# Kernel tuning notes

Measured on AMD Instinct MI355X. Metric: run time of the kernel, lower is better.

Reference implementation:

```python
import jax, jax.numpy as jnp
import numpy as np

B, L, D = 4, 256, 2048
LE, DE = 2048, 1024
H = 16
HD = D // H  # 128
ROPE_BASE = 10000.0


def apply_rope(q):
    # q: [B, H, L, HD]; rotate interleaved pairs along seq axis L (torchtune-style)
    half = HD // 2
    inv_freq = 1.0 / (ROPE_BASE ** (jnp.arange(0, HD, 2, dtype=jnp.float32) / HD))  # [half]
    pos = jnp.arange(L, dtype=jnp.float32)
    ang = pos[:, None] * inv_freq[None, :]           # [L, half]
    cos = jnp.cos(ang)[None, None, :, :]             # [1,1,L,half]
    sin = jnp.sin(ang)[None, None, :, :]
    qr = q.reshape(B, H, L, half, 2)
    q1, q2 = qr[..., 0], qr[..., 1]
    out = jnp.stack([q1 * cos - q2 * sin, q1 * sin + q2 * cos], axis=-1)
    return out.reshape(B, H, L, HD)


def setup_inputs() -> dict:
    key = jax.random.key(0)
    ks = jax.random.split(key, 7)
    s_d = 1.0 / np.sqrt(D)
    s_e = 1.0 / np.sqrt(DE)
    return {
        "x": jax.random.normal(ks[0], (B, L, D), jnp.float32),
        "encoder_inputs": jax.random.normal(ks[1], (B, LE, DE), jnp.float32),
        "Wq": jax.random.normal(ks[2], (D, D), jnp.float32) * s_d,
        "bq": jnp.zeros((D,), jnp.float32),
        "Wk": jax.random.normal(ks[3], (DE, D), jnp.float32) * s_e,
        "bk": jnp.zeros((D,), jnp.float32),
        "Wv": jax.random.normal(ks[4], (DE, D), jnp.float32) * s_e,
        "bv": jnp.zeros((D,), jnp.float32),
        "Wo": jax.random.normal(ks[5], (D, D), jnp.float32) * s_d,
        "bo": jnp.zeros((D,), jnp.float32),
    }


def reference(x, encoder_inputs, Wq, bq, Wk, bk, Wv, bv, Wo, bo):
    q = (x @ Wq + bq).reshape(B, L, H, HD).transpose(0, 2, 1, 3)              # [B,H,L,HD]
    k = (encoder_inputs @ Wk + bk).reshape(B, LE, H, HD).transpose(0, 2, 1, 3)  # [B,H,Le,HD]
    v = (encoder_inputs @ Wv + bv).reshape(B, LE, H, HD).transpose(0, 2, 1, 3)
    q = apply_rope(q)
    scale = 1.0 / jnp.sqrt(jnp.float32(HD))
    scores = jnp.einsum("bhld,bhmd->bhlm", q, k) * scale                      # [B,H,L,Le]
    attn = jax.nn.softmax(scores, axis=-1)
    ctx = jnp.einsum("bhlm,bhmd->bhld", attn, v)                              # [B,H,L,HD]
    ctx = ctx.transpose(0, 2, 1, 3).reshape(B, L, D)
    return ctx @ Wo + bo
```

## Files before the change

### kernel.cpp

```cpp
#include <hip/hip_runtime.h>


#define B_ 4
#define L_ 256
#define D_ 2048
#define LE_ 2048
#define DE_ 1024
#define H_ 16
#define HD_ 128

using f32x4  = __attribute__((ext_vector_type(4))) float;
using bf16x8 = __attribute__((ext_vector_type(8))) short;

__device__ __forceinline__ unsigned short f2bf(float f) {
    union { float f; unsigned int u; } v; v.f = f;
    unsigned int r = v.u + 0x7fffu + ((v.u >> 16) & 1u);
    return (unsigned short)(r >> 16);
}
__device__ __forceinline__ float b2f(unsigned short h) {
    union { unsigned int u; float f; } v; v.u = ((unsigned int)h) << 16;
    return v.f;
}

__device__ __forceinline__ void load_lds16(const void* g, void* l) {
    __builtin_amdgcn_global_load_lds((const __attribute__((address_space(1))) void*)g,
                                     (__attribute__((address_space(3))) void*)l, 16, 0, 0);
}

__global__ void cast_f32_bf16(const float* __restrict__ in, unsigned short* __restrict__ out, int n) {
    int i = (blockIdx.x * 256 + threadIdx.x) * 4;
    if (i < n) {
        float4 v = *(const float4*)(in + i);
        ushort4 o;
        o.x = f2bf(v.x); o.y = f2bf(v.y); o.z = f2bf(v.z); o.w = f2bf(v.w);
        *(ushort4*)(out + i) = o;
    }
}

__global__ void transpose_f32_bf16(const float* __restrict__ in, unsigned short* __restrict__ out,
                                   int R, int C) {
    __shared__ float t[32][33];
    int r0 = blockIdx.y * 32, c0 = blockIdx.x * 32;
    int tx = threadIdx.x, ty = threadIdx.y;
    #pragma unroll
    for (int i = 0; i < 32; i += 8) t[ty + i][tx] = in[(long)(r0 + ty + i) * C + c0 + tx];
    __syncthreads();
    #pragma unroll
    for (int i = 0; i < 32; i += 8) out[(long)(c0 + ty + i) * R + r0 + tx] = f2bf(t[tx][ty + i]);
}

__global__ void transpose_bf16_batched(const unsigned short* __restrict__ in,
                                       unsigned short* __restrict__ out, int R, int C) {
    __shared__ unsigned short t[32][33];
    long zo = (long)blockIdx.z * R * C;
    int r0 = blockIdx.y * 32, c0 = blockIdx.x * 32;
    int tx = threadIdx.x, ty = threadIdx.y;
    #pragma unroll
    for (int i = 0; i < 32; i += 8) t[ty + i][tx] = in[zo + (long)(r0 + ty + i) * C + c0 + tx];
    __syncthreads();
    #pragma unroll
    for (int i = 0; i < 32; i += 8) out[zo + (long)(c0 + ty + i) * R + r0 + tx] = t[tx][ty + i];
}

__global__ void combine_q_rope(const float* __restrict__ P, const float* __restrict__ bq,
                               unsigned short* __restrict__ Q) {
    int gid = blockIdx.x * 256 + threadIdx.x;
    int p = gid & 63;
    int h = (gid >> 6) & 15;
    int m = gid >> 10;
    int n = h * 128 + 2 * p;
    long i0 = (long)m * 2048 + n;
    float q1 = bq[n], q2 = bq[n + 1];
    #pragma unroll
    for (int pt = 0; pt < 4; pt++) {
        float2 a = *(const float2*)(P + (long)pt * 2097152 + i0);
        q1 += a.x; q2 += a.y;
    }
    int l = m & 255, b = m >> 8;
    float inv = powf(10000.0f, -(float)p * (1.0f / 64.0f));
    float s, c;
    sincosf((float)l * inv, &s, &c);
    const float sc = 0.08838834764831845f;
    long qi = (((long)(b * 16 + h) * 256 + l) << 7) + 2 * p;
    ushort2 o;
    o.x = f2bf((q1 * c - q2 * s) * sc);
    o.y = f2bf((q1 * s + q2 * c) * sc);
    *(ushort2*)(Q + qi) = o;
}

__global__ void combine_pv(const float* __restrict__ P, unsigned short* __restrict__ ctx) {
    int gid = blockIdx.x * 256 + threadIdx.x;
    long e = (long)gid * 4;
    float4 a = *(const float4*)(P + e);
    #pragma unroll
    for (int pt = 1; pt < 4; pt++) {
        float4 b = *(const float4*)(P + (long)pt * 2097152 + e);
        a.x += b.x; a.y += b.y; a.z += b.z; a.w += b.w;
    }
    int bh = (int)(e >> 15);
    int m  = (int)((e >> 7) & 255);
    int d  = (int)(e & 127);
    int bb = bh >> 4, h = bh & 15;
    ushort4 o;
    o.x = f2bf(a.x); o.y = f2bf(a.y); o.z = f2bf(a.z); o.w = f2bf(a.w);
    *(ushort4*)(ctx + ((long)(bb * 256 + m)) * 2048 + h * 128 + d) = o;
}

__global__ void combine_o(const float* __restrict__ P, const float* __restrict__ bo,
                          float* __restrict__ out) {
    int gid = blockIdx.x * 256 + threadIdx.x;
    long e = (long)gid * 4;
    int n = (int)(e & 2047);
    float4 r = *(const float4*)(bo + n);
    #pragma unroll
    for (int pt = 0; pt < 4; pt++) {
        float4 a = *(const float4*)(P + (long)pt * 2097152 + e);
        r.x += a.x; r.y += a.y; r.z += a.z; r.w += a.w;
    }
    *(float4*)(out + e) = r;
}

__launch_bounds__(256)
__global__ void softmax_rows(unsigned short* __restrict__ S) {
    long row = blockIdx.x;
    unsigned short* p = S + row * 2048;
    int t = threadIdx.x, w = t >> 6, lane = t & 63;
    bf16x8 raw = *(const bf16x8*)(p + t * 8);
    float v[8];
    float mx = -1e30f;
    #pragma unroll
    for (int i = 0; i < 8; i++) { v[i] = b2f((unsigned short)raw[i]); mx = fmaxf(mx, v[i]); }
    #pragma unroll
    for (int o = 32; o; o >>= 1) mx = fmaxf(mx, __shfl_xor(mx, o));
    __shared__ float redm[4], reds[4];
    if (lane == 0) redm[w] = mx;
    __syncthreads();
    mx = fmaxf(fmaxf(redm[0], redm[1]), fmaxf(redm[2], redm[3]));
    float sum = 0.f;
    #pragma unroll
    for (int i = 0; i < 8; i++) { v[i] = __expf(v[i] - mx); sum += v[i]; }
    #pragma unroll
    for (int o = 32; o; o >>= 1) sum += __shfl_xor(sum, o);
    if (lane == 0) reds[w] = sum;
    __syncthreads();
    sum = reds[0] + reds[1] + reds[2] + reds[3];
    float r = 1.0f / sum;
    bf16x8 res;
    #pragma unroll
    for (int i = 0; i < 8; i++) res[i] = (short)f2bf(v[i] * r);
    *(bf16x8*)(p + t * 8) = res;
}

template <int EPI>
__launch_bounds__(256)
__global__ void gemm_bt(const unsigned short* __restrict__ A, const unsigned short* __restrict__ Bt,
                        const float* __restrict__ biasA, const float* __restrict__ biasB,
                        void* __restrict__ outA, void* __restrict__ outB,
                        int M, int N, int K, int lda, int ldb,
                        long strideA, long strideB, int zdiv, int nsplit) {
    __shared__ __align__(16) unsigned short smem[24576];
    const int z = blockIdx.z;
    int s = 0, bh = z;
    if constexpr (EPI == 4) { s = z / zdiv; bh = z - s * zdiv; }
    const unsigned short* Ab = A + (long)bh * strideA + (long)s * K;
    const unsigned short* Bb = Bt + (long)bh * strideB + (long)s * K;
    const int m0 = blockIdx.y * 128, n0 = blockIdx.x * 128;
    const int tid = threadIdx.x;
    const int w = tid >> 6, lane = tid & 63;
    const int quad = lane >> 4, l16 = lane & 15;
    const int wr = w >> 1, wc = w & 1;
    const int srow = lane >> 2;
    const int scol = (lane & 3) * 8;

    f32x4 acc[4][4] = {};

    auto stage = [&](int k0, int p) {
        unsigned short* As = smem + p * 8192;
        unsigned short* Bs = As + 4096;
        #pragma unroll
        for (int q = 0; q < 2; q++) {
            int ci = q * 4 + w;
            int row = ci * 16 + srow;
            load_lds16(Ab + (long)(m0 + row) * lda + k0 + scol, (void*)(As + ci * 512));
            load_lds16(Bb + (long)(n0 + row) * ldb + k0 + scol, (void*)(Bs + ci * 512));
        }
    };

    const int nk = K >> 5;
    stage(0, 0);
    stage(32, 1);
    int p = 0;
    for (int i = 0; i < nk; i++) {
        if (i + 1 < nk) asm volatile("s_waitcnt vmcnt(4)" ::: "memory");
        else            asm volatile("s_waitcnt vmcnt(0)" ::: "memory");
        __builtin_amdgcn_s_barrier();
        if (i + 2 < nk) {
            int pn = p + 2; if (pn >= 3) pn -= 3;
            stage((i + 2) << 5, pn);
        }
        const unsigned short* As = smem + p * 8192;
        const unsigned short* Bs = As + 4096;
        bf16x8 af[4], bfr[4];
        #pragma unroll
        for (int ii = 0; ii < 4; ii++) {
            int r = wr * 64 + ii * 16 + l16;
            af[ii] = *(const bf16x8*)(As + r * 32 + quad * 8);
        }
        #pragma unroll
        for (int j = 0; j < 4; j++) {
            int r = wc * 64 + j * 16 + l16;
            bfr[j] = *(const bf16x8*)(Bs + r * 32 + quad * 8);
        }
        #pragma unroll
        for (int ii = 0; ii < 4; ii++)
            #pragma unroll
            for (int j = 0; j < 4; j++)
                acc[ii][j] = __builtin_amdgcn_mfma_f32_16x16x32_bf16(af[ii], bfr[j], acc[ii][j], 0, 0, 0);
        if (++p >= 3) p -= 3;
    }
    __syncthreads();

    if constexpr (EPI == 1 || EPI == 2) {
        const bool second = (EPI == 1) && (n0 >= nsplit);
        const float* bias = second ? biasB : biasA;
        const int n0e = second ? n0 - nsplit : n0;
        unsigned short* dst = (unsigned short*)(second ? outB : outA);
        #pragma unroll
        for (int pp = 0; pp < 2; pp++) {
            if (wr == pp) {
                #pragma unroll
                for (int i = 0; i < 4; i++)
                    #pragma unroll
                    for (int j = 0; j < 4; j++)
                        #pragma unroll
                        for (int r = 0; r < 4; r++) {
                            int ml = i * 16 + quad * 4 + r;
                            int n  = wc * 64 + j * 16 + l16;
                            float v = acc[i][j][r];
                            if (bias) v += bias[n0e + n];
                            smem[ml * 136 + n] = f2bf(v);
                        }
            }
            __syncthreads();
            #pragma unroll
            for (int pass = 0; pass < 4; pass++) {
                int row = pass * 16 + (tid >> 4);
                int seg = tid & 15;
                bf16x8 val = *(const bf16x8*)(smem + row * 136 + seg * 8);
                int m = m0 + pp * 64 + row;
                if constexpr (EPI == 1) {
                    int h = n0e >> 7;
                    int b = m >> 11, mrow = m & 2047;
                    long idx = (((long)(b * 16 + h)) << 11) + mrow;
                    *(bf16x8*)(dst + (idx << 7) + seg * 8) = val;
                } else {
                    *(bf16x8*)((unsigned short*)outA + (long)z * M * N + (long)m * N + n0 + seg * 8) = val;
                }
            }
            __syncthreads();
        }
    } else {
        float* smf = (float*)smem;
        long zo = ((long)s * zdiv + bh) * (long)M * N;
        #pragma unroll
        for (int q4 = 0; q4 < 4; q4++) {
            if (wr == (q4 >> 1)) {
                #pragma unroll
                for (int ii = 0; ii < 2; ii++) {
                    int i = (q4 & 1) * 2 + ii;
                    #pragma unroll
                    for (int j = 0; j < 4; j++)
                        #pragma unroll
                        for (int r = 0; r < 4; r++) {
                            int ml = ii * 16 + quad * 4 + r;
                            int n  = wc * 64 + j * 16 + l16;
                            smf[ml * 132 + n] = acc[i][j][r];
                        }
                }
            }
            __syncthreads();
            #pragma unroll
            for (int pass = 0; pass < 4; pass++) {
                int row = pass * 8 + (tid >> 5);
                int seg = tid & 31;
                float4 val = *(const float4*)(smf + row * 132 + seg * 4);
                int m = m0 + q4 * 32 + row;
                *(float4*)((float*)outA + zo + (long)m * N + n0 + seg * 4) = val;
            }
            __syncthreads();
        }
    }
}

extern "C" void kernel_launch(void* const* d_in, const int* in_sizes, int n_in,
                              void* d_out, int out_size, void* d_ws, size_t ws_size,
                              hipStream_t stream) {
    const float* x   = (const float*)d_in[0];
    const float* enc = (const float*)d_in[1];
    const float* Wq  = (const float*)d_in[2];
    const float* bq  = (const float*)d_in[3];
    const float* Wk  = (const float*)d_in[4];
    const float* bk  = (const float*)d_in[5];
    const float* Wv  = (const float*)d_in[6];
    const float* bv  = (const float*)d_in[7];
    const float* Wo  = (const float*)d_in[8];
    const float* bo  = (const float*)d_in[9];
    float* out = (float*)d_out;

    char* ws = (char*)d_ws;
    const size_t MB = 1024 * 1024;
    unsigned short* x_bf   = (unsigned short*)(ws + 0 * MB);
    unsigned short* enc_bf = (unsigned short*)(ws + 4 * MB);
    unsigned short* WqT    = (unsigned short*)(ws + 20 * MB);
    unsigned short* WkvT   = (unsigned short*)(ws + 28 * MB);
    unsigned short* V_bf   = (unsigned short*)(ws + 36 * MB);
    unsigned short* K_bf   = (unsigned short*)(ws + 68 * MB);
    unsigned short* WoT    = (unsigned short*)(ws + 100 * MB);
    unsigned short* Q_bf   = (unsigned short*)(ws + 108 * MB);
    unsigned short* Vt     = (unsigned short*)(ws + 112 * MB);
    unsigned short* S_bf   = (unsigned short*)(ws + 0 * MB);
    float*          Pq     = (float*)(ws + 36 * MB);
    float*          Ppv    = (float*)(ws + 68 * MB);
    float*          Po     = (float*)(ws + 0 * MB);
    unsigned short* ctx_bf = (unsigned short*)(ws + 108 * MB);

    dim3 tb(32, 8);

    cast_f32_bf16<<<2048, 256, 0, stream>>>(x, x_bf, 2097152);
    cast_f32_bf16<<<8192, 256, 0, stream>>>(enc, enc_bf, 8388608);

    transpose_f32_bf16<<<dim3(64, 64), tb, 0, stream>>>(Wq, WqT, 2048, 2048);
    transpose_f32_bf16<<<dim3(64, 32), tb, 0, stream>>>(Wk, WkvT, 1024, 2048);
    transpose_f32_bf16<<<dim3(64, 32), tb, 0, stream>>>(Wv, WkvT + 2048 * 1024, 1024, 2048);
    transpose_f32_bf16<<<dim3(64, 64), tb, 0, stream>>>(Wo, WoT, 2048, 2048);

    gemm_bt<4><<<dim3(16, 8, 4), 256, 0, stream>>>(x_bf, WqT, nullptr, nullptr, Pq, nullptr,
                                                   1024, 2048, 512, 2048, 2048, 0, 0, 1, 0);
    combine_q_rope<<<4096, 256, 0, stream>>>(Pq, bq, Q_bf);

    gemm_bt<1><<<dim3(32, 64, 1), 256, 0, stream>>>(enc_bf, WkvT, bk, bv, K_bf, V_bf,
                                                    8192, 4096, 1024, 1024, 1024, 0, 0, 1, 2048);

    transpose_bf16_batched<<<dim3(4, 64, 64), tb, 0, stream>>>(V_bf, Vt, 2048, 128);

    gemm_bt<2><<<dim3(16, 2, 64), 256, 0, stream>>>(Q_bf, K_bf, nullptr, nullptr, S_bf, nullptr,
                                                    256, 2048, 128, 128, 128,
                                                    256 * 128, 2048 * 128, 1, 0);
    softmax_rows<<<16384, 256, 0, stream>>>(S_bf);

    gemm_bt<4><<<dim3(1, 2, 256), 256, 0, stream>>>(S_bf, Vt, nullptr, nullptr, Ppv, nullptr,
                                                    256, 128, 512, 2048, 2048,
                                                    256 * 2048, 128 * 2048, 64, 0);
    combine_pv<<<2048, 256, 0, stream>>>(Ppv, ctx_bf);

    gemm_bt<4><<<dim3(16, 8, 4), 256, 0, stream>>>(ctx_bf, WoT, nullptr, nullptr, Po, nullptr,
                                                   1024, 2048, 512, 2048, 2048, 0, 0, 1, 0);
    combine_o<<<2048, 256, 0, stream>>>(Po, bo, out);
}
```

Measured before the change: 406.0 us.

## Fuse V transpose into dedicated KV projection GEMM with larger tiles

```diff
diff --git a/kernel.cpp b/kernel.cpp
--- a/kernel.cpp
+++ b/kernel.cpp
@@ -47,19 +47,6 @@
     __syncthreads();
     #pragma unroll
     for (int i = 0; i < 32; i += 8) out[(long)(c0 + ty + i) * R + r0 + tx] = f2bf(t[tx][ty + i]);
-}
-
-__global__ void transpose_bf16_batched(const unsigned short* __restrict__ in,
-                                       unsigned short* __restrict__ out, int R, int C) {
-    __shared__ unsigned short t[32][33];
-    long zo = (long)blockIdx.z * R * C;
-    int r0 = blockIdx.y * 32, c0 = blockIdx.x * 32;
-    int tx = threadIdx.x, ty = threadIdx.y;
-    #pragma unroll
-    for (int i = 0; i < 32; i += 8) t[ty + i][tx] = in[zo + (long)(r0 + ty + i) * C + c0 + tx];
-    __syncthreads();
-    #pragma unroll
-    for (int i = 0; i < 32; i += 8) out[zo + (long)(c0 + ty + i) * R + r0 + tx] = t[tx][ty + i];
 }
 
 __global__ void combine_q_rope(const float* __restrict__ P, const float* __restrict__ bq,
@@ -151,14 +138,131 @@
     *(bf16x8*)(p + t * 8) = res;
 }
 
+__launch_bounds__(512, 6)
+__global__ void gemm_kv(const unsigned short* __restrict__ A, const unsigned short* __restrict__ Bt,
+                        const float* __restrict__ bk, const float* __restrict__ bv,
+                        unsigned short* __restrict__ Kout, unsigned short* __restrict__ Vt) {
+    __shared__ __align__(16) unsigned short smem[24576];
+    const int lda = 1024, ldb = 1024, K = 1024;
+    const int m0 = blockIdx.y * 256, n0 = blockIdx.x * 128;
+    const int tid = threadIdx.x;
+    const int w = tid >> 6, lane = tid & 63;
+    const int quad = lane >> 4, l16 = lane & 15;
+    const int wrow = w >> 1, wcol = w & 1;
+    const int srow = lane >> 2;
+    const int scol = (lane & 3) * 8;
+
+    f32x4 acc[4][4] = {};
+
+    auto stage = [&](int k0, int p) {
+        unsigned short* base = smem + p * 12288;
+        #pragma unroll
+        for (int q = 0; q < 3; q++) {
+            int ci = w * 3 + q;
+            unsigned short* l = base + ci * 512;
+            const unsigned short* g;
+            if (ci < 16) g = A  + (long)(m0 + ci * 16 + srow) * lda + k0 + scol;
+            else         g = Bt + (long)(n0 + (ci - 16) * 16 + srow) * ldb + k0 + scol;
+            load_lds16(g, l);
+        }
+    };
+
+    const int nk = K >> 5;
+    stage(0, 0);
+    for (int i = 0; i < nk; i++) {
+        __syncthreads();
+        if (i + 1 < nk) stage((i + 1) << 5, (i + 1) & 1);
+        const unsigned short* As = smem + (i & 1) * 12288;
+        const unsigned short* Bs = As + 8192;
+        bf16x8 af[4], bfr[4];
+        #pragma unroll
+        for (int ii = 0; ii < 4; ii++) {
+            int r = wrow * 64 + ii * 16 + l16;
+            af[ii] = *(const bf16x8*)(As + r * 32 + quad * 8);
+        }
+        #pragma unroll
+        for (int j = 0; j < 4; j++) {
+            int r = wcol * 64 + j * 16 + l16;
+            bfr[j] = *(const bf16x8*)(Bs + r * 32 + quad * 8);
+        }
+        #pragma unroll
+        for (int ii = 0; ii < 4; ii++)
+            #pragma unroll
+            for (int j = 0; j < 4; j++)
+                acc[ii][j] = __builtin_amdgcn_mfma_f32_16x16x32_bf16(af[ii], bfr[j], acc[ii][j], 0, 0, 0);
+    }
+    __syncthreads();
+
+    const int b = m0 >> 11;
+    if (n0 < 2048) {
+        const int h = n0 >> 7;
+        #pragma unroll
+        for (int qq = 0; qq < 4; qq++) {
+            if (wrow == qq) {
+                #pragma unroll
+                for (int i = 0; i < 4; i++)
+                    #pragma unroll
+                    for (int j = 0; j < 4; j++)
+                        #pragma unroll
+                        for (int r = 0; r < 4; r++) {
+                            int ml = i * 16 + quad * 4 + r;
+                            int n  = wcol * 64 + j * 16 + l16;
+                            smem[ml * 136 + n] = f2bf(acc[i][j][r] + bk[n0 + n]);
+                        }
+            }
+            __syncthreads();
+            #pragma unroll
+            for (int pass = 0; pass < 2; pass++) {
+                int row = pass * 32 + (tid >> 4);
+                int seg = tid & 15;
+                bf16x8 val = *(const bf16x8*)(smem + row * 136 + seg * 8);
+                int m = m0 + qq * 64 + row;
+                int le = m & 2047;
+                long idx = (((long)(b * 16 + h)) << 11) + le;
+                *(bf16x8*)(Kout + (idx << 7) + seg * 8) = val;
+            }
+            __syncthreads();
+        }
+    } else {
+        const int n0e = n0 - 2048;
+        const int h = n0e >> 7;
+        unsigned short* vbase = Vt + ((long)(b * 16 + h)) * (128 * 2048);
+        #pragma unroll
+        for (int qq = 0; qq < 4; qq++) {
+            if (wrow == qq) {
+                #pragma unroll
+                for (int i = 0; i < 4; i++)
+                    #pragma unroll
+                    for (int j = 0; j < 4; j++) {
+                        int d = wcol * 64 + j * 16 + l16;
+                        #pragma unroll
+                        for (int r = 0; r < 4; r++) {
+                            int ml = i * 16 + quad * 4 + r;
+                            smem[d * 72 + ml] = f2bf(acc[i][j][r] + bv[n0e + d]);
+                        }
+                    }
+            }
+            __syncthreads();
+            #pragma unroll
+            for (int pass = 0; pass < 4; pass++) {
+                int d = pass * 32 + (tid >> 4);
+                int c = tid & 15;
+                ushort4 val = *(const ushort4*)(smem + d * 72 + c * 4);
+                int le = (m0 & 2047) + qq * 64 + c * 4;
+                *(ushort4*)(vbase + (long)d * 2048 + le) = val;
+            }
+            __syncthreads();
+        }
+    }
+}
+
 template <int EPI>
 __launch_bounds__(256)
 __global__ void gemm_bt(const unsigned short* __restrict__ A, const unsigned short* __restrict__ Bt,
-                        const float* __restrict__ biasA, const float* __restrict__ biasB,
-                        void* __restrict__ outA, void* __restrict__ outB,
+                        void* __restrict__ outA,
                         int M, int N, int K, int lda, int ldb,
-                        long strideA, long strideB, int zdiv, int nsplit) {
-    __shared__ __align__(16) unsigned short smem[24576];
+                        long strideA, long strideB, int zdiv) {
+    __shared__ __align__(16) unsigned short smem[16384];
     const int z = blockIdx.z;
     int s = 0, bh = z;
     if constexpr (EPI == 4) { s = z / zdiv; bh = z - s * zdiv; }
@@ -188,17 +292,10 @@
 
     const int nk = K >> 5;
     stage(0, 0);
-    stage(32, 1);
-    int p = 0;
     for (int i = 0; i < nk; i++) {
-        if (i + 1 < nk) asm volatile("s_waitcnt vmcnt(4)" ::: "memory");
-        else            asm volatile("s_waitcnt vmcnt(0)" ::: "memory");
-        __builtin_amdgcn_s_barrier();
-        if (i + 2 < nk) {
-            int pn = p + 2; if (pn >= 3) pn -= 3;
-            stage((i + 2) << 5, pn);
-        }
-        const unsigned short* As = smem + p * 8192;
+        __syncthreads();
+        if (i + 1 < nk) stage((i + 1) << 5, (i + 1) & 1);
+        const unsigned short* As = smem + (i & 1) * 8192;
         const unsigned short* Bs = As + 4096;
         bf16x8 af[4], bfr[4];
         #pragma unroll
@@ -216,15 +313,10 @@
             #pragma unroll
             for (int j = 0; j < 4; j++)
                 acc[ii][j] = __builtin_amdgcn_mfma_f32_16x16x32_bf16(af[ii], bfr[j], acc[ii][j], 0, 0, 0);
-        if (++p >= 3) p -= 3;
     }
     __syncthreads();
 
-    if constexpr (EPI == 1 || EPI == 2) {
-        const bool second = (EPI == 1) && (n0 >= nsplit);
-        const float* bias = second ? biasB : biasA;
-        const int n0e = second ? n0 - nsplit : n0;
-        unsigned short* dst = (unsigned short*)(second ? outB : outA);
+    if constexpr (EPI == 2) {
         #pragma unroll
         for (int pp = 0; pp < 2; pp++) {
             if (wr == pp) {
@@ -236,9 +328,7 @@
                         for (int r = 0; r < 4; r++) {
                             int ml = i * 16 + quad * 4 + r;
                             int n  = wc * 64 + j * 16 + l16;
-                            float v = acc[i][j][r];
-                            if (bias) v += bias[n0e + n];
-                            smem[ml * 136 + n] = f2bf(v);
+                            smem[ml * 136 + n] = f2bf(acc[i][j][r]);
                         }
             }
             __syncthreads();
@@ -248,14 +338,7 @@
                 int seg = tid & 15;
                 bf16x8 val = *(const bf16x8*)(smem + row * 136 + seg * 8);
                 int m = m0 + pp * 64 + row;
-                if constexpr (EPI == 1) {
-                    int h = n0e >> 7;
-                    int b = m >> 11, mrow = m & 2047;
-                    long idx = (((long)(b * 16 + h)) << 11) + mrow;
-                    *(bf16x8*)(dst + (idx << 7) + seg * 8) = val;
-                } else {
-                    *(bf16x8*)((unsigned short*)outA + (long)z * M * N + (long)m * N + n0 + seg * 8) = val;
-                }
+                *(bf16x8*)((unsigned short*)outA + (long)z * M * N + (long)m * N + n0 + seg * 8) = val;
             }
             __syncthreads();
         }
@@ -313,7 +396,6 @@
     unsigned short* enc_bf = (unsigned short*)(ws + 4 * MB);
     unsigned short* WqT    = (unsigned short*)(ws + 20 * MB);
     unsigned short* WkvT   = (unsigned short*)(ws + 28 * MB);
-    unsigned short* V_bf   = (unsigned short*)(ws + 36 * MB);
     unsigned short* K_bf   = (unsigned short*)(ws + 68 * MB);
     unsigned short* WoT    = (unsigned short*)(ws + 100 * MB);
     unsigned short* Q_bf   = (unsigned short*)(ws + 108 * MB);
@@ -334,26 +416,23 @@
     transpose_f32_bf16<<<dim3(64, 32), tb, 0, stream>>>(Wv, WkvT + 2048 * 1024, 1024, 2048);
     transpose_f32_bf16<<<dim3(64, 64), tb, 0, stream>>>(Wo, WoT, 2048, 2048);
 
-    gemm_bt<4><<<dim3(16, 8, 4), 256, 0, stream>>>(x_bf, WqT, nullptr, nullptr, Pq, nullptr,
-                                                   1024, 2048, 512, 2048, 2048, 0, 0, 1, 0);
+    gemm_bt<4><<<dim3(16, 8, 4), 256, 0, stream>>>(x_bf, WqT, Pq,
+                                                   1024, 2048, 512, 2048, 2048, 0, 0, 1);
     combine_q_rope<<<4096, 256, 0, stream>>>(Pq, bq, Q_bf);
 
-    gemm_bt<1><<<dim3(32, 64, 1), 256, 0, stream>>>(enc_bf, WkvT, bk, bv, K_bf, V_bf,
-                                                    8192, 4096, 1024, 1024, 1024, 0, 0, 1, 2048);
-
-    transpose_bf16_batched<<<dim3(4, 64, 64), tb, 0, stream>>>(V_bf, Vt, 2048, 128);
-
-    gemm_bt<2><<<dim3(16, 2, 64), 256, 0, stream>>>(Q_bf, K_bf, nullptr, nullptr, S_bf, nullptr,
+    gemm_kv<<<dim3(32, 32, 1), 512, 0, stream>>>(enc_bf, WkvT, bk, bv, K_bf, Vt);
+
+    gemm_bt<2><<<dim3(16, 2, 64), 256, 0, stream>>>(Q_bf, K_bf, S_bf,
                                                     256, 2048, 128, 128, 128,
-                                                    256 * 128, 2048 * 128, 1, 0);
+                                                    256 * 128, 2048 * 128, 1);
     softmax_rows<<<16384, 256, 0, stream>>>(S_bf);
 
-    gemm_bt<4><<<dim3(1, 2, 256), 256, 0, stream>>>(S_bf, Vt, nullptr, nullptr, Ppv, nullptr,
+    gemm_bt<4><<<dim3(1, 2, 256), 256, 0, stream>>>(S_bf, Vt, Ppv,
                                                     256, 128, 512, 2048, 2048,
-                                                    256 * 2048, 128 * 2048, 64, 0);
+                                                    256 * 2048, 128 * 2048, 64);
     combine_pv<<<2048, 256, 0, stream>>>(Ppv, ctx_bf);
 
-    gemm_bt<4><<<dim3(16, 8, 4), 256, 0, stream>>>(ctx_bf, WoT, nullptr, nullptr, Po, nullptr,
-                                                   1024, 2048, 512, 2048, 2048, 0, 0, 1, 0);
+    gemm_bt<4><<<dim3(16, 8, 4), 256, 0, stream>>>(ctx_bf, WoT, Po,
+                                                   1024, 2048, 512, 2048, 2048, 0, 0, 1);
     combine_o<<<2048, 256, 0, stream>>>(Po, bo, out);
 }
```

New measurement: 614.2 us. +51.3%, slower.
